# Kernel tuning notes

Hardware: AMD Instinct MI355X
Metric: run time of the kernel (lower is better)

Reference implementation:

```python
import jax, jax.numpy as jnp
import numpy as np

N_NODES = 50000
N_EDGES = 800000
IN_CH = 128
OUT_CH = 64
HID_CH = 2 * OUT_CH  # 128


def gcn_conv(x, edge_index, W, b, n_nodes):
    """PyG GCNConv: linear -> add self-loops -> sym-normalized scatter-add -> bias."""
    h = x @ W  # [N, out]
    loop = jnp.arange(n_nodes)
    row = jnp.concatenate([edge_index[0], loop])  # source nodes
    col = jnp.concatenate([edge_index[1], loop])  # target nodes
    deg = jax.ops.segment_sum(jnp.ones_like(col, dtype=h.dtype), col, num_segments=n_nodes)
    dinv = jnp.where(deg > 0, jax.lax.rsqrt(jnp.maximum(deg, 1.0)), 0.0)
    norm = dinv[row] * dinv[col]  # [E+N]
    msg = h[row] * norm[:, None]  # gather + scale, [E+N, out]
    out = jax.ops.segment_sum(msg, col, num_segments=n_nodes)  # scatter-add
    return out + b


def setup_inputs() -> dict:
    key = jax.random.key(0)
    ks = jax.random.split(key, 9)
    x = jax.random.normal(ks[0], (N_NODES, IN_CH), dtype=jnp.float32)
    edge_index = jax.random.randint(ks[1], (2, N_EDGES), 0, N_NODES, dtype=jnp.int64)
    s_in = 1.0 / np.sqrt(IN_CH)
    s_hid = 1.0 / np.sqrt(HID_CH)
    W1 = jax.random.normal(ks[2], (IN_CH, HID_CH), dtype=jnp.float32) * s_in
    b1 = jnp.zeros((HID_CH,), dtype=jnp.float32)
    W2 = jax.random.normal(ks[3], (HID_CH, OUT_CH), dtype=jnp.float32) * s_hid
    b2 = jnp.zeros((OUT_CH,), dtype=jnp.float32)
    W3 = jax.random.normal(ks[4], (HID_CH, OUT_CH), dtype=jnp.float32) * s_hid
    b3 = jnp.zeros((OUT_CH,), dtype=jnp.float32)
    return {"x": x, "edge_index": edge_index, "W1": W1, "b1": b1,
            "W2": W2, "b2": b2, "W3": W3, "b3": b3}


def reference(x, edge_index, W1, b1, W2, b2, W3, b3):
    act = jax.nn.relu
    hidden = act(gcn_conv(x, edge_index, W1, b1, N_NODES))
    x1 = act(gcn_conv(hidden, edge_index, W2, b2, N_NODES))
    x2 = act(gcn_conv(hidden, edge_index, W3, b3, N_NODES))
    return (x1, x2)
```

## Files before the change

### kernel.cpp

```cpp
#include <hip/hip_runtime.h>

#define N_NODES 50000
#define N_EDGES 800000
#define CH 128
#define SCAN_BLKS 98
#define WT_PAD 136
#define DUMMY N_NODES
#define AGG_HALF_BLKS 1563

typedef __attribute__((ext_vector_type(8))) short short8;
typedef __attribute__((ext_vector_type(4))) float floatx4;

__device__ __forceinline__ short f2bf(float f) {
    union { float f; unsigned u; } v; v.f = f;
    unsigned r = v.u + 0x7fff + ((v.u >> 16) & 1);
    return (short)(r >> 16);
}
__device__ __forceinline__ float bflo(unsigned u) {
    union { unsigned u; float f; } v; v.u = u << 16; return v.f;
}
__device__ __forceinline__ float bfhi(unsigned u) {
    union { unsigned u; float f; } v; v.u = u & 0xffff0000u; return v.f;
}


__global__ __launch_bounds__(256) void prep_kernel(const float* __restrict__ W1,
                                                   const float* __restrict__ W2,
                                                   const float* __restrict__ W3,
                                                   const float* __restrict__ b2,
                                                   const float* __restrict__ b3,
                                                   unsigned short* __restrict__ Wt1,
                                                   unsigned short* __restrict__ Wt23,
                                                   float* __restrict__ b23,
                                                   int* __restrict__ counts,
                                                   unsigned int* __restrict__ gdummy) {
    int i = blockIdx.x * blockDim.x + threadIdx.x;
    if (i < 128 * 128) {
        int n = i >> 7, k = i & 127;
        Wt1[i] = (unsigned short)f2bf(W1[k * 128 + n]);
        float w = (n < 64) ? W2[k * 64 + n] : W3[k * 64 + (n - 64)];
        Wt23[i] = (unsigned short)f2bf(w);
    } else if (i < 128 * 128 + 128) {
        int k2 = i - 128 * 128;
        b23[k2] = (k2 < 64) ? b2[k2] : b3[k2 - 64];
    } else if (i < 128 * 128 + 192) {
        gdummy[i - (128 * 128 + 128)] = 0;
    }
    for (int j = i; j < N_NODES; j += 66 * 256) counts[j] = 0;
}


__global__ void rank_kernel(const int* __restrict__ ei, int* __restrict__ counts,
                            int* __restrict__ rank) {
    int e = blockIdx.x * blockDim.x + threadIdx.x;
    if (e < N_EDGES) rank[e] = atomicAdd(&counts[ei[N_EDGES + e]], 1);
}

__global__ __launch_bounds__(256) void scan_block_kernel(const int* __restrict__ counts,
                                                         int* __restrict__ row_ptr,
                                                         float* __restrict__ dinv,
                                                         int* __restrict__ bsum) {
    __shared__ int s[256];
    int tid = threadIdx.x;
    int base = blockIdx.x * 512;
    int i0 = base + 2 * tid, i1 = i0 + 1;
    int v0 = (i0 < N_NODES) ? counts[i0] : 0;
    int v1 = (i1 < N_NODES) ? counts[i1] : 0;
    if (i0 < N_NODES) dinv[i0] = rsqrtf((float)(v0 + 1));
    if (i1 < N_NODES) dinv[i1] = rsqrtf((float)(v1 + 1));
    int p0 = (v0 + 3) & ~3, p1 = (v1 + 3) & ~3;
    int t = p0 + p1;
    s[tid] = t;
    __syncthreads();
    for (int off = 1; off < 256; off <<= 1) {
        int tmp = (tid >= off) ? s[tid - off] : 0;
        __syncthreads();
        s[tid] += tmp;
        __syncthreads();
    }
    int pre = s[tid] - t;
    if (i0 < N_NODES) row_ptr[i0] = pre;
    if (i1 < N_NODES) row_ptr[i1] = pre + p0;
    if (tid == 255) bsum[blockIdx.x] = s[255];
}

__global__ __launch_bounds__(256) void scan_fix_kernel(int* __restrict__ row_ptr,
                                                       const int* __restrict__ bsum,
                                                       const int* __restrict__ degs,
                                                       unsigned short* __restrict__ sorted_src) {
    __shared__ int s[128];
    int tid = threadIdx.x;
    if (tid < 128) s[tid] = (tid < SCAN_BLKS) ? bsum[tid] : 0;
    __syncthreads();
    for (int off = 1; off < 128; off <<= 1) {
        int t = (tid < 128 && tid >= off) ? s[tid - off] : 0;
        __syncthreads();
        if (tid < 128) s[tid] += t;
        __syncthreads();
    }
    int blockoff = (blockIdx.x == 0) ? 0 : s[blockIdx.x - 1];
    int base = blockIdx.x * 512;
    for (int i = base + tid; i < base + 512; i += 256) {
        if (i < N_NODES) {
            int v = row_ptr[i] + blockoff;
            row_ptr[i] = v;
            int d = degs[i];
            int pc = (d + 3) & ~3;
            for (int p = v + d; p < v + pc; ++p) sorted_src[p] = (unsigned short)DUMMY;
        }
    }
}

__global__ void scatter_plain(const int* __restrict__ ei, const int* __restrict__ row_ptr,
                              const int* __restrict__ rank,
                              unsigned short* __restrict__ sorted_src) {
    int e = blockIdx.x * blockDim.x + threadIdx.x;
    if (e < N_EDGES) {
        int dst = ei[N_EDGES + e];
        sorted_src[row_ptr[dst] + rank[e]] = (unsigned short)ei[e];
    }
}


template <bool A_BF16>
__global__ __launch_bounds__(256) void gemm_mfma(const void* __restrict__ Ain,
                                                 const unsigned short* __restrict__ Wt,
                                                 const float* __restrict__ dinv,
                                                 unsigned short* __restrict__ g) {
    __shared__ unsigned short lds[128 * WT_PAD];
    int tid = threadIdx.x;
    int wave = tid >> 6, lane = tid & 63;
    int quad = lane >> 4, ln = lane & 15;

    {
        int r = tid >> 1, h = tid & 1;
        const int4* src = (const int4*)(Wt + r * 128 + h * 64);
#pragma unroll
        for (int i = 0; i < 8; ++i)
            *(int4*)&lds[r * WT_PAD + h * 64 + i * 8] = src[i];
    }

    int row_base = blockIdx.x * 64 + wave * 16;
    int arow = row_base + ln;
    bool ok = arow < N_NODES;
    short8 afrag[4];
    if (A_BF16) {
        const unsigned short* A = (const unsigned short*)Ain;
#pragma unroll
        for (int kk = 0; kk < 4; ++kk) {
            short8 v = {};
            if (ok) v = *(const short8*)(A + arow * 128 + kk * 32 + quad * 8);
            afrag[kk] = v;
        }
    } else {
        const float* A = (const float*)Ain;
#pragma unroll
        for (int kk = 0; kk < 4; ++kk) {
            short8 v = {};
            if (ok) {
                const float* p = A + arow * 128 + kk * 32 + quad * 8;
#pragma unroll
                for (int j = 0; j < 8; ++j) v[j] = f2bf(p[j]);
            }
            afrag[kk] = v;
        }
    }
    __syncthreads();

    floatx4 acc[8] = {};
#pragma unroll
    for (int n0 = 0; n0 < 8; ++n0) {
#pragma unroll
        for (int kk = 0; kk < 4; ++kk) {
            short8 b = *(const short8*)&lds[(n0 * 16 + ln) * WT_PAD + kk * 32 + quad * 8];
            acc[n0] = __builtin_amdgcn_mfma_f32_16x16x32_bf16(afrag[kk], b, acc[n0], 0, 0, 0);
        }
    }

    __syncthreads();
    unsigned short* st = &lds[wave * 16 * WT_PAD];
    float dv[4];
#pragma unroll
    for (int r = 0; r < 4; ++r) {
        int node = row_base + quad * 4 + r;
        dv[r] = (node < N_NODES) ? dinv[node] : 0.f;
    }
#pragma unroll
    for (int n0 = 0; n0 < 8; ++n0)
#pragma unroll
        for (int r = 0; r < 4; ++r)
            st[(quad * 4 + r) * WT_PAD + n0 * 16 + ln] =
                (unsigned short)f2bf(acc[n0][r] * dv[r]);
    __syncthreads();

#pragma unroll
    for (int i = 0; i < 4; ++i) {
        int row = i * 4 + quad;
        int node = row_base + row;
        short8 v = *(const short8*)&st[row * WT_PAD + ln * 8];
        if (node < N_NODES) *(short8*)(g + node * 128 + ln * 8) = v;
    }
}


template <int MODE>
__global__ __launch_bounds__(256) void aggregate_bf16(const unsigned short* __restrict__ g,
                                                      const float* __restrict__ dinv,
                                                      const int* __restrict__ row_ptr,
                                                      const int* __restrict__ degs,
                                                      const unsigned short* __restrict__ srcs,
                                                      const float* __restrict__ bias,
                                                      void* __restrict__ outp) {
    int h = 0, nb = blockIdx.x;
    if (nb >= AGG_HALF_BLKS) { h = 1; nb -= AGG_HALF_BLKS; }
    int n = nb * 32 + (threadIdx.x >> 3);
    if (n >= N_NODES) return;
    int c4 = threadIdx.x & 7;
    int hoff = h * 8;
    const uint4* grow = (const uint4*)g;
    uint4 u = grow[n * 16 + hoff + c4];
    float a0 = bflo(u.x), a1 = bfhi(u.x), a2 = bflo(u.y), a3 = bfhi(u.y);
    float a4 = bflo(u.z), a5 = bfhi(u.z), a6 = bflo(u.w), a7 = bfhi(u.w);
    float c0 = 0.f, c1 = 0.f, c2 = 0.f, c3 = 0.f, c5 = 0.f, c6 = 0.f, c7 = 0.f, c8 = 0.f;
    int beg = row_ptr[n];
    int pend = beg + ((degs[n] + 3) & ~3);
    int e = beg;
    for (; e + 8 <= pend; e += 8) {
        ushort4 sa = *(const ushort4*)&srcs[e];
        ushort4 sb = *(const ushort4*)&srcs[e + 4];
        uint4 v0 = grow[sa.x * 16 + hoff + c4];
        uint4 v1 = grow[sa.y * 16 + hoff + c4];
        uint4 v2 = grow[sa.z * 16 + hoff + c4];
        uint4 v3 = grow[sa.w * 16 + hoff + c4];
        uint4 v4 = grow[sb.x * 16 + hoff + c4];
        uint4 v5 = grow[sb.y * 16 + hoff + c4];
        uint4 v6 = grow[sb.z * 16 + hoff + c4];
        uint4 v7 = grow[sb.w * 16 + hoff + c4];
        a0 += bflo(v0.x); a1 += bfhi(v0.x); a2 += bflo(v0.y); a3 += bfhi(v0.y);
        a4 += bflo(v0.z); a5 += bfhi(v0.z); a6 += bflo(v0.w); a7 += bfhi(v0.w);
        c0 += bflo(v1.x); c1 += bfhi(v1.x); c2 += bflo(v1.y); c3 += bfhi(v1.y);
        c5 += bflo(v1.z); c6 += bfhi(v1.z); c7 += bflo(v1.w); c8 += bfhi(v1.w);
        a0 += bflo(v2.x); a1 += bfhi(v2.x); a2 += bflo(v2.y); a3 += bfhi(v2.y);
        a4 += bflo(v2.z); a5 += bfhi(v2.z); a6 += bflo(v2.w); a7 += bfhi(v2.w);
        c0 += bflo(v3.x); c1 += bfhi(v3.x); c2 += bflo(v3.y); c3 += bfhi(v3.y);
        c5 += bflo(v3.z); c6 += bfhi(v3.z); c7 += bflo(v3.w); c8 += bfhi(v3.w);
        a0 += bflo(v4.x); a1 += bfhi(v4.x); a2 += bflo(v4.y); a3 += bfhi(v4.y);
        a4 += bflo(v4.z); a5 += bfhi(v4.z); a6 += bflo(v4.w); a7 += bfhi(v4.w);
        c0 += bflo(v5.x); c1 += bfhi(v5.x); c2 += bflo(v5.y); c3 += bfhi(v5.y);
        c5 += bflo(v5.z); c6 += bfhi(v5.z); c7 += bflo(v5.w); c8 += bfhi(v5.w);
        a0 += bflo(v6.x); a1 += bfhi(v6.x); a2 += bflo(v6.y); a3 += bfhi(v6.y);
        a4 += bflo(v6.z); a5 += bfhi(v6.z); a6 += bflo(v6.w); a7 += bfhi(v6.w);
        c0 += bflo(v7.x); c1 += bfhi(v7.x); c2 += bflo(v7.y); c3 += bfhi(v7.y);
        c5 += bflo(v7.z); c6 += bfhi(v7.z); c7 += bflo(v7.w); c8 += bfhi(v7.w);
    }
    if (e < pend) {
        ushort4 sa = *(const ushort4*)&srcs[e];
        uint4 v0 = grow[sa.x * 16 + hoff + c4];
        uint4 v1 = grow[sa.y * 16 + hoff + c4];
        uint4 v2 = grow[sa.z * 16 + hoff + c4];
        uint4 v3 = grow[sa.w * 16 + hoff + c4];
        a0 += bflo(v0.x); a1 += bfhi(v0.x); a2 += bflo(v0.y); a3 += bfhi(v0.y);
        a4 += bflo(v0.z); a5 += bfhi(v0.z); a6 += bflo(v0.w); a7 += bfhi(v0.w);
        c0 += bflo(v1.x); c1 += bfhi(v1.x); c2 += bflo(v1.y); c3 += bfhi(v1.y);
        c5 += bflo(v1.z); c6 += bfhi(v1.z); c7 += bflo(v1.w); c8 += bfhi(v1.w);
        a0 += bflo(v2.x); a1 += bfhi(v2.x); a2 += bflo(v2.y); a3 += bfhi(v2.y);
        a4 += bflo(v2.z); a5 += bfhi(v2.z); a6 += bflo(v2.w); a7 += bfhi(v2.w);
        c0 += bflo(v3.x); c1 += bfhi(v3.x); c2 += bflo(v3.y); c3 += bfhi(v3.y);
        c5 += bflo(v3.z); c6 += bfhi(v3.z); c7 += bflo(v3.w); c8 += bfhi(v3.w);
    }
    a0 += c0; a1 += c1; a2 += c2; a3 += c3; a4 += c5; a5 += c6; a6 += c7; a7 += c8;
    float d = dinv[n];
    float4 bv0 = ((const float4*)bias)[h * 16 + c4 * 2];
    float4 bv1 = ((const float4*)bias)[h * 16 + c4 * 2 + 1];
    float o0 = fmaxf(d * a0 + bv0.x, 0.f);
    float o1 = fmaxf(d * a1 + bv0.y, 0.f);
    float o2 = fmaxf(d * a2 + bv0.z, 0.f);
    float o3 = fmaxf(d * a3 + bv0.w, 0.f);
    float o4 = fmaxf(d * a4 + bv1.x, 0.f);
    float o5 = fmaxf(d * a5 + bv1.y, 0.f);
    float o6 = fmaxf(d * a6 + bv1.z, 0.f);
    float o7 = fmaxf(d * a7 + bv1.w, 0.f);
    if (MODE == 0) {
        uint4 w;
        w.x = ((unsigned)(unsigned short)f2bf(o0)) | (((unsigned)(unsigned short)f2bf(o1)) << 16);
        w.y = ((unsigned)(unsigned short)f2bf(o2)) | (((unsigned)(unsigned short)f2bf(o3)) << 16);
        w.z = ((unsigned)(unsigned short)f2bf(o4)) | (((unsigned)(unsigned short)f2bf(o5)) << 16);
        w.w = ((unsigned)(unsigned short)f2bf(o6)) | (((unsigned)(unsigned short)f2bf(o7)) << 16);
        ((uint4*)outp)[n * 16 + hoff + c4] = w;
    } else {
        float* out = (float*)outp + (size_t)h * N_NODES * 64;
        ((float4*)out)[n * 16 + c4 * 2] = make_float4(o0, o1, o2, o3);
        ((float4*)out)[n * 16 + c4 * 2 + 1] = make_float4(o4, o5, o6, o7);
    }
}


extern "C" void kernel_launch(void* const* d_in, const int* in_sizes, int n_in,
                              void* d_out, int out_size, void* d_ws, size_t ws_size,
                              hipStream_t stream) {
    const float* x  = (const float*)d_in[0];
    const int*   ei = (const int*)d_in[1];
    const float* W1 = (const float*)d_in[2];
    const float* b1 = (const float*)d_in[3];
    const float* W2 = (const float*)d_in[4];
    const float* b2 = (const float*)d_in[5];
    const float* W3 = (const float*)d_in[6];
    const float* b3 = (const float*)d_in[7];
    float* out = (float*)d_out;

    char* w = (char*)d_ws;
    int*            counts     = (int*)(w + 0);
    int*            row_ptr    = (int*)(w + 204800);
    float*          dinv       = (float*)(w + 409600);
    int*            rank       = (int*)(w + 614400);
    unsigned short* sorted_src = (unsigned short*)(w + 3814400);
    unsigned short* Wt1        = (unsigned short*)(w + 7614400);
    unsigned short* Wt23       = (unsigned short*)(w + 7647168);
    float*          b23        = (float*)(w + 7679936);
    int*            bsum       = (int*)(w + 7680448);
    unsigned short* g1         = (unsigned short*)(w + 8388608);
    unsigned short* hidden     = (unsigned short*)(w + 22020096);

    prep_kernel<<<66, 256, 0, stream>>>(W1, W2, W3, b2, b3, Wt1, Wt23, b23, counts,
                                        (unsigned int*)(g1 + N_NODES * 128));
    rank_kernel<<<(N_EDGES + 255) / 256, 256, 0, stream>>>(ei, counts, rank);
    scan_block_kernel<<<SCAN_BLKS, 256, 0, stream>>>(counts, row_ptr, dinv, bsum);
    scan_fix_kernel<<<SCAN_BLKS, 256, 0, stream>>>(row_ptr, bsum, counts, sorted_src);
    scatter_plain<<<(N_EDGES + 255) / 256, 256, 0, stream>>>(ei, row_ptr, rank, sorted_src);

    const int gemm_blocks = (N_NODES + 63) / 64;
    const int agg_blocks = 2 * AGG_HALF_BLKS;

    gemm_mfma<false><<<gemm_blocks, 256, 0, stream>>>(x, Wt1, dinv, g1);
    aggregate_bf16<0><<<agg_blocks, 256, 0, stream>>>(g1, dinv, row_ptr, counts, sorted_src, b1, hidden);

    gemm_mfma<true><<<gemm_blocks, 256, 0, stream>>>(hidden, Wt23, dinv, g1);
    aggregate_bf16<1><<<agg_blocks, 256, 0, stream>>>(g1, dinv, row_ptr, counts, sorted_src, b23, out);
}
```

Measured before the change: 217.3 us.

## Fuse layer-1 aggregation with layer-2/3 GEMM and split final aggregation into quarters

The first aggregation now writes its ReLU'd bf16 hidden rows into an LDS tile, and the same block immediately runs the MFMA GEMM against the combined W2|W3 weights. This removes the hidden tensor's global write and re-read and drops one kernel launch. The final aggregation is split over a 2D grid of 32-channel quarters with 4 threads per node. The fused kernel uses 4 threads per node with 32 float accumulators each and a simple 2-edge loop, which raises register pressure and lowers gather parallelism compared with the former 8-edge unrolled loop.

New measurement: 245.4 us. +12.9%, slower.

```diff
diff --git a/kernel.cpp b/kernel.cpp
--- a/kernel.cpp
+++ b/kernel.cpp
@@ -6,7 +6,6 @@
 #define SCAN_BLKS 98
 #define WT_PAD 136
 #define DUMMY N_NODES
-#define AGG_HALF_BLKS 1563
 
 typedef __attribute__((ext_vector_type(8))) short short8;
 typedef __attribute__((ext_vector_type(4))) float floatx4;
@@ -21,6 +20,15 @@
 }
 __device__ __forceinline__ float bfhi(unsigned u) {
     union { unsigned u; float f; } v; v.u = u & 0xffff0000u; return v.f;
+}
+__device__ __forceinline__ unsigned packbf(float a, float b) {
+    return ((unsigned)(unsigned short)f2bf(a)) | (((unsigned)(unsigned short)f2bf(b)) << 16);
+}
+__device__ __forceinline__ void acc8(float* a, uint4 v) {
+    a[0] += bflo(v.x); a[1] += bfhi(v.x);
+    a[2] += bflo(v.y); a[3] += bfhi(v.y);
+    a[4] += bflo(v.z); a[5] += bfhi(v.z);
+    a[6] += bflo(v.w); a[7] += bfhi(v.w);
 }
 
 
@@ -33,7 +41,8 @@
                                                    unsigned short* __restrict__ Wt23,
                                                    float* __restrict__ b23,
                                                    int* __restrict__ counts,
-                                                   unsigned int* __restrict__ gdummy) {
+                                                   unsigned int* __restrict__ g1dummy,
+                                                   unsigned int* __restrict__ g2dummy) {
     int i = blockIdx.x * blockDim.x + threadIdx.x;
     if (i < 128 * 128) {
         int n = i >> 7, k = i & 127;
@@ -44,7 +53,9 @@
         int k2 = i - 128 * 128;
         b23[k2] = (k2 < 64) ? b2[k2] : b3[k2 - 64];
     } else if (i < 128 * 128 + 192) {
-        gdummy[i - (128 * 128 + 128)] = 0;
+        g1dummy[i - (128 * 128 + 128)] = 0;
+    } else if (i < 128 * 128 + 256) {
+        g2dummy[i - (128 * 128 + 192)] = 0;
     }
     for (int j = i; j < N_NODES; j += 66 * 256) counts[j] = 0;
 }
@@ -122,11 +133,10 @@
 }
 
 
-template <bool A_BF16>
-__global__ __launch_bounds__(256) void gemm_mfma(const void* __restrict__ Ain,
-                                                 const unsigned short* __restrict__ Wt,
-                                                 const float* __restrict__ dinv,
-                                                 unsigned short* __restrict__ g) {
+__global__ __launch_bounds__(256) void gemm_mfma_f32(const float* __restrict__ A,
+                                                     const unsigned short* __restrict__ Wt,
+                                                     const float* __restrict__ dinv,
+                                                     unsigned short* __restrict__ g) {
     __shared__ unsigned short lds[128 * WT_PAD];
     int tid = threadIdx.x;
     int wave = tid >> 6, lane = tid & 63;
@@ -144,26 +154,15 @@
     int arow = row_base + ln;
     bool ok = arow < N_NODES;
     short8 afrag[4];
-    if (A_BF16) {
-        const unsigned short* A = (const unsigned short*)Ain;
-#pragma unroll
-        for (int kk = 0; kk < 4; ++kk) {
-            short8 v = {};
-            if (ok) v = *(const short8*)(A + arow * 128 + kk * 32 + quad * 8);
-            afrag[kk] = v;
-        }
-    } else {
-        const float* A = (const float*)Ain;
-#pragma unroll
-        for (int kk = 0; kk < 4; ++kk) {
-            short8 v = {};
-            if (ok) {
-                const float* p = A + arow * 128 + kk * 32 + quad * 8;
-#pragma unroll
-                for (int j = 0; j < 8; ++j) v[j] = f2bf(p[j]);
-            }
-            afrag[kk] = v;
-        }
+#pragma unroll
+    for (int kk = 0; kk < 4; ++kk) {
+        short8 v = {};
+        if (ok) {
+            const float* p = A + arow * 128 + kk * 32 + quad * 8;
+#pragma unroll
+            for (int j = 0; j < 8; ++j) v[j] = f2bf(p[j]);
+        }
+        afrag[kk] = v;
     }
     __syncthreads();
 
@@ -203,95 +202,181 @@
 }
 
 
-template <int MODE>
-__global__ __launch_bounds__(256) void aggregate_bf16(const unsigned short* __restrict__ g,
+__global__ __launch_bounds__(256) void agg_gemm_fused(const unsigned short* __restrict__ g1,
                                                       const float* __restrict__ dinv,
                                                       const int* __restrict__ row_ptr,
                                                       const int* __restrict__ degs,
                                                       const unsigned short* __restrict__ srcs,
-                                                      const float* __restrict__ bias,
-                                                      void* __restrict__ outp) {
-    int h = 0, nb = blockIdx.x;
-    if (nb >= AGG_HALF_BLKS) { h = 1; nb -= AGG_HALF_BLKS; }
-    int n = nb * 32 + (threadIdx.x >> 3);
+                                                      const float* __restrict__ b1,
+                                                      const unsigned short* __restrict__ Wt23,
+                                                      unsigned short* __restrict__ g2) {
+    __shared__ unsigned short wlds[128 * WT_PAD];
+    __shared__ unsigned short atile[64 * WT_PAD];
+    int tid = threadIdx.x;
+
+    {
+        int r = tid >> 1, h = tid & 1;
+        const int4* src = (const int4*)(Wt23 + r * 128 + h * 64);
+#pragma unroll
+        for (int i = 0; i < 8; ++i)
+            *(int4*)&wlds[r * WT_PAD + h * 64 + i * 8] = src[i];
+    }
+
+    int slot = tid >> 2;
+    int part = tid & 3;
+    int n = blockIdx.x * 64 + slot;
+    unsigned short* arow = &atile[slot * WT_PAD + part * 32];
+    if (n < N_NODES) {
+        const uint4* grow = (const uint4*)g1;
+        const uint4* gr = grow + (size_t)n * 16 + part * 4;
+        float acc[32];
+        {
+            uint4 u0 = gr[0], u1 = gr[1], u2 = gr[2], u3 = gr[3];
+#pragma unroll
+            for (int j = 0; j < 32; ++j) acc[j] = 0.f;
+            acc8(acc, u0); acc8(acc + 8, u1); acc8(acc + 16, u2); acc8(acc + 24, u3);
+        }
+        int beg = row_ptr[n];
+        int pend = beg + ((degs[n] + 3) & ~3);
+        for (int e = beg; e < pend; e += 2) {
+            ushort2 ss = *(const ushort2*)&srcs[e];
+            const uint4* p0 = grow + (size_t)ss.x * 16 + part * 4;
+            const uint4* p1 = grow + (size_t)ss.y * 16 + part * 4;
+            uint4 va0 = p0[0], va1 = p0[1], va2 = p0[2], va3 = p0[3];
+            uint4 vb0 = p1[0], vb1 = p1[1], vb2 = p1[2], vb3 = p1[3];
+            acc8(acc, va0); acc8(acc + 8, va1); acc8(acc + 16, va2); acc8(acc + 24, va3);
+            acc8(acc, vb0); acc8(acc + 8, vb1); acc8(acc + 16, vb2); acc8(acc + 24, vb3);
+        }
+        float d = dinv[n];
+        const float4* bb = (const float4*)b1 + part * 8;
+        unsigned wbuf[16];
+#pragma unroll
+        for (int j = 0; j < 8; ++j) {
+            float4 b = bb[j];
+            float o0 = fmaxf(d * acc[4 * j + 0] + b.x, 0.f);
+            float o1 = fmaxf(d * acc[4 * j + 1] + b.y, 0.f);
+            float o2 = fmaxf(d * acc[4 * j + 2] + b.z, 0.f);
+            float o3 = fmaxf(d * acc[4 * j + 3] + b.w, 0.f);
+            wbuf[2 * j] = packbf(o0, o1);
+            wbuf[2 * j + 1] = packbf(o2, o3);
+        }
+#pragma unroll
+        for (int j = 0; j < 4; ++j)
+            *(int4*)(arow + j * 8) = *(const int4*)&wbuf[j * 4];
+    } else {
+        int4 z = {0, 0, 0, 0};
+#pragma unroll
+        for (int j = 0; j < 4; ++j) *(int4*)(arow + j * 8) = z;
+    }
+    __syncthreads();
+
+    int wave = tid >> 6, lane = tid & 63;
+    int quad = lane >> 4, ln = lane & 15;
+    int row_base = blockIdx.x * 64 + wave * 16;
+    short8 afrag[4];
+#pragma unroll
+    for (int kk = 0; kk < 4; ++kk)
+        afrag[kk] = *(const short8*)&atile[(wave * 16 + ln) * WT_PAD + kk * 32 + quad * 8];
+
+    floatx4 acc2[8] = {};
+#pragma unroll
+    for (int n0 = 0; n0 < 8; ++n0) {
+#pragma unroll
+        for (int kk = 0; kk < 4; ++kk) {
+            short8 b = *(const short8*)&wlds[(n0 * 16 + ln) * WT_PAD + kk * 32 + quad * 8];
+            acc2[n0] = __builtin_amdgcn_mfma_f32_16x16x32_bf16(afrag[kk], b, acc2[n0], 0, 0, 0);
+        }
+    }
+
+    __syncthreads();
+    unsigned short* st = &wlds[wave * 16 * WT_PAD];
+    float dv[4];
+#pragma unroll
+    for (int r = 0; r < 4; ++r) {
+        int node = row_base + quad * 4 + r;
+        dv[r] = (node < N_NODES) ? dinv[node] : 0.f;
+    }
+#pragma unroll
+    for (int n0 = 0; n0 < 8; ++n0)
+#pragma unroll
+        for (int r = 0; r < 4; ++r)
+            st[(quad * 4 + r) * WT_PAD + n0 * 16 + ln] =
+                (unsigned short)f2bf(acc2[n0][r] * dv[r]);
+    __syncthreads();
+
+#pragma unroll
+    for (int i = 0; i < 4; ++i) {
+        int row = i * 4 + quad;
+        int node = row_base + row;
+        short8 v = *(const short8*)&st[row * WT_PAD + ln * 8];
+        if (node < N_NODES) *(short8*)(g2 + node * 128 + ln * 8) = v;
+    }
+}
+
+
+__global__ __launch_bounds__(256) void aggregate_q(const unsigned short* __restrict__ g,
+                                                   const float* __restrict__ dinv,
+                                                   const int* __restrict__ row_ptr,
+                                                   const int* __restrict__ degs,
+                                                   const unsigned short* __restrict__ srcs,
+                                                   const float* __restrict__ bias,
+                                                   float* __restrict__ out) {
+    int q = blockIdx.y;
+    int n = blockIdx.x * 64 + (threadIdx.x >> 2);
     if (n >= N_NODES) return;
-    int c4 = threadIdx.x & 7;
-    int hoff = h * 8;
+    int c4 = threadIdx.x & 3;
+    int qoff = q * 4 + c4;
     const uint4* grow = (const uint4*)g;
-    uint4 u = grow[n * 16 + hoff + c4];
-    float a0 = bflo(u.x), a1 = bfhi(u.x), a2 = bflo(u.y), a3 = bfhi(u.y);
-    float a4 = bflo(u.z), a5 = bfhi(u.z), a6 = bflo(u.w), a7 = bfhi(u.w);
-    float c0 = 0.f, c1 = 0.f, c2 = 0.f, c3 = 0.f, c5 = 0.f, c6 = 0.f, c7 = 0.f, c8 = 0.f;
+    float a[8], c[8];
+    {
+        uint4 u = grow[(size_t)n * 16 + qoff];
+        a[0] = bflo(u.x); a[1] = bfhi(u.x); a[2] = bflo(u.y); a[3] = bfhi(u.y);
+        a[4] = bflo(u.z); a[5] = bfhi(u.z); a[6] = bflo(u.w); a[7] = bfhi(u.w);
+#pragma unroll
+        for (int j = 0; j < 8; ++j) c[j] = 0.f;
+    }
     int beg = row_ptr[n];
     int pend = beg + ((degs[n] + 3) & ~3);
     int e = beg;
     for (; e + 8 <= pend; e += 8) {
         ushort4 sa = *(const ushort4*)&srcs[e];
         ushort4 sb = *(const ushort4*)&srcs[e + 4];
-        uint4 v0 = grow[sa.x * 16 + hoff + c4];
-        uint4 v1 = grow[sa.y * 16 + hoff + c4];
-        uint4 v2 = grow[sa.z * 16 + hoff + c4];
-        uint4 v3 = grow[sa.w * 16 + hoff + c4];
-        uint4 v4 = grow[sb.x * 16 + hoff + c4];
-        uint4 v5 = grow[sb.y * 16 + hoff + c4];
-        uint4 v6 = grow[sb.z * 16 + hoff + c4];
-        uint4 v7 = grow[sb.w * 16 + hoff + c4];
-        a0 += bflo(v0.x); a1 += bfhi(v0.x); a2 += bflo(v0.y); a3 += bfhi(v0.y);
-        a4 += bflo(v0.z); a5 += bfhi(v0.z); a6 += bflo(v0.w); a7 += bfhi(v0.w);
-        c0 += bflo(v1.x); c1 += bfhi(v1.x); c2 += bflo(v1.y); c3 += bfhi(v1.y);
-        c5 += bflo(v1.z); c6 += bfhi(v1.z); c7 += bflo(v1.w); c8 += bfhi(v1.w);
-        a0 += bflo(v2.x); a1 += bfhi(v2.x); a2 += bflo(v2.y); a3 += bfhi(v2.y);
-        a4 += bflo(v2.z); a5 += bfhi(v2.z); a6 += bflo(v2.w); a7 += bfhi(v2.w);
-        c0 += bflo(v3.x); c1 += bfhi(v3.x); c2 += bflo(v3.y); c3 += bfhi(v3.y);
-        c5 += bflo(v3.z); c6 += bfhi(v3.z); c7 += bflo(v3.w); c8 += bfhi(v3.w);
-        a0 += bflo(v4.x); a1 += bfhi(v4.x); a2 += bflo(v4.y); a3 += bfhi(v4.y);
-        a4 += bflo(v4.z); a5 += bfhi(v4.z); a6 += bflo(v4.w); a7 += bfhi(v4.w);
-        c0 += bflo(v5.x); c1 += bfhi(v5.x); c2 += bflo(v5.y); c3 += bfhi(v5.y);
-        c5 += bflo(v5.z); c6 += bfhi(v5.z); c7 += bflo(v5.w); c8 += bfhi(v5.w);
-        a0 += bflo(v6.x); a1 += bfhi(v6.x); a2 += bflo(v6.y); a3 += bfhi(v6.y);
-        a4 += bflo(v6.z); a5 += bfhi(v6.z); a6 += bflo(v6.w); a7 += bfhi(v6.w);
-        c0 += bflo(v7.x); c1 += bfhi(v7.x); c2 += bflo(v7.y); c3 += bfhi(v7.y);
-        c5 += bflo(v7.z); c6 += bfhi(v7.z); c7 += bflo(v7.w); c8 += bfhi(v7.w);
+        uint4 v0 = grow[(size_t)sa.x * 16 + qoff];
+        uint4 v1 = grow[(size_t)sa.y * 16 + qoff];
+        uint4 v2 = grow[(size_t)sa.z * 16 + qoff];
+        uint4 v3 = grow[(size_t)sa.w * 16 + qoff];
+        uint4 v4 = grow[(size_t)sb.x * 16 + qoff];
+        uint4 v5 = grow[(size_t)sb.y * 16 + qoff];
+        uint4 v6 = grow[(size_t)sb.z * 16 + qoff];
+        uint4 v7 = grow[(size_t)sb.w * 16 + qoff];
+        acc8(a, v0); acc8(c, v1); acc8(a, v2); acc8(c, v3);
+        acc8(a, v4); acc8(c, v5); acc8(a, v6); acc8(c, v7);
     }
     if (e < pend) {
         ushort4 sa = *(const ushort4*)&srcs[e];
-        uint4 v0 = grow[sa.x * 16 + hoff + c4];
-        uint4 v1 = grow[sa.y * 16 + hoff + c4];
-        uint4 v2 = grow[sa.z * 16 + hoff + c4];
-        uint4 v3 = grow[sa.w * 16 + hoff + c4];
-        a0 += bflo(v0.x); a1 += bfhi(v0.x); a2 += bflo(v0.y); a3 += bfhi(v0.y);
-        a4 += bflo(v0.z); a5 += bfhi(v0.z); a6 += bflo(v0.w); a7 += bfhi(v0.w);
-        c0 += bflo(v1.x); c1 += bfhi(v1.x); c2 += bflo(v1.y); c3 += bfhi(v1.y);
-        c5 += bflo(v1.z); c6 += bfhi(v1.z); c7 += bflo(v1.w); c8 += bfhi(v1.w);
-        a0 += bflo(v2.x); a1 += bfhi(v2.x); a2 += bflo(v2.y); a3 += bfhi(v2.y);
-        a4 += bflo(v2.z); a5 += bfhi(v2.z); a6 += bflo(v2.w); a7 += bfhi(v2.w);
-        c0 += bflo(v3.x); c1 += bfhi(v3.x); c2 += bflo(v3.y); c3 += bfhi(v3.y);
-        c5 += bflo(v3.z); c6 += bfhi(v3.z); c7 += bflo(v3.w); c8 += bfhi(v3.w);
-    }
-    a0 += c0; a1 += c1; a2 += c2; a3 += c3; a4 += c5; a5 += c6; a6 += c7; a7 += c8;
+        uint4 v0 = grow[(size_t)sa.x * 16 + qoff];
+        uint4 v1 = grow[(size_t)sa.y * 16 + qoff];
+        uint4 v2 = grow[(size_t)sa.z * 16 + qoff];
+        uint4 v3 = grow[(size_t)sa.w * 16 + qoff];
+        acc8(a, v0); acc8(c, v1); acc8(a, v2); acc8(c, v3);
+    }
+#pragma unroll
+    for (int j = 0; j < 8; ++j) a[j] += c[j];
     float d = dinv[n];
-    float4 bv0 = ((const float4*)bias)[h * 16 + c4 * 2];
-    float4 bv1 = ((const float4*)bias)[h * 16 + c4 * 2 + 1];
-    float o0 = fmaxf(d * a0 + bv0.x, 0.f);
-    float o1 = fmaxf(d * a1 + bv0.y, 0.f);
-    float o2 = fmaxf(d * a2 + bv0.z, 0.f);
-    float o3 = fmaxf(d * a3 + bv0.w, 0.f);
-    float o4 = fmaxf(d * a4 + bv1.x, 0.f);
-    float o5 = fmaxf(d * a5 + bv1.y, 0.f);
-    float o6 = fmaxf(d * a6 + bv1.z, 0.f);
-    float o7 = fmaxf(d * a7 + bv1.w, 0.f);
-    if (MODE == 0) {
-        uint4 w;
-        w.x = ((unsigned)(unsigned short)f2bf(o0)) | (((unsigned)(unsigned short)f2bf(o1)) << 16);
-        w.y = ((unsigned)(unsigned short)f2bf(o2)) | (((unsigned)(unsigned short)f2bf(o3)) << 16);
-        w.z = ((unsigned)(unsigned short)f2bf(o4)) | (((unsigned)(unsigned short)f2bf(o5)) << 16);
-        w.w = ((unsigned)(unsigned short)f2bf(o6)) | (((unsigned)(unsigned short)f2bf(o7)) << 16);
-        ((uint4*)outp)[n * 16 + hoff + c4] = w;
-    } else {
-        float* out = (float*)outp + (size_t)h * N_NODES * 64;
-        ((float4*)out)[n * 16 + c4 * 2] = make_float4(o0, o1, o2, o3);
-        ((float4*)out)[n * 16 + c4 * 2 + 1] = make_float4(o4, o5, o6, o7);
-    }
+    float4 bv0 = ((const float4*)bias)[q * 8 + c4 * 2];
+    float4 bv1 = ((const float4*)bias)[q * 8 + c4 * 2 + 1];
+    float4 p0, p1;
+    p0.x = fmaxf(d * a[0] + bv0.x, 0.f);
+    p0.y = fmaxf(d * a[1] + bv0.y, 0.f);
+    p0.z = fmaxf(d * a[2] + bv0.z, 0.f);
+    p0.w = fmaxf(d * a[3] + bv0.w, 0.f);
+    p1.x = fmaxf(d * a[4] + bv1.x, 0.f);
+    p1.y = fmaxf(d * a[5] + bv1.y, 0.f);
+    p1.z = fmaxf(d * a[6] + bv1.z, 0.f);
+    p1.w = fmaxf(d * a[7] + bv1.w, 0.f);
+    float* ob = out + (size_t)(q >> 1) * N_NODES * 64 + n * 64 + (q & 1) * 32 + c4 * 8;
+    *(float4*)ob = p0;
+    *(float4*)(ob + 4) = p1;
 }
 
 
@@ -319,21 +404,23 @@
     float*          b23        = (float*)(w + 7679936);
     int*            bsum       = (int*)(w + 7680448);
     unsigned short* g1         = (unsigned short*)(w + 8388608);
-    unsigned short* hidden     = (unsigned short*)(w + 22020096);
+    unsigned short* g2         = (unsigned short*)(w + 22020096);
 
     prep_kernel<<<66, 256, 0, stream>>>(W1, W2, W3, b2, b3, Wt1, Wt23, b23, counts,
-                                        (unsigned int*)(g1 + N_NODES * 128));
+                                        (unsigned int*)(g1 + N_NODES * 128),
+                                        (unsigned int*)(g2 + N_NODES * 128));
     rank_kernel<<<(N_EDGES + 255) / 256, 256, 0, stream>>>(ei, counts, rank);
     scan_block_kernel<<<SCAN_BLKS, 256, 0, stream>>>(counts, row_ptr, dinv, bsum);
     scan_fix_kernel<<<SCAN_BLKS, 256, 0, stream>>>(row_ptr, bsum, counts, sorted_src);
     scatter_plain<<<(N_EDGES + 255) / 256, 256, 0, stream>>>(ei, row_ptr, rank, sorted_src);
 
-    const int gemm_blocks = (N_NODES + 63) / 64;
-    const int agg_blocks = 2 * AGG_HALF_BLKS;
-
-    gemm_mfma<false><<<gemm_blocks, 256, 0, stream>>>(x, Wt1, dinv, g1);
-    aggregate_bf16<0><<<agg_blocks, 256, 0, stream>>>(g1, dinv, row_ptr, counts, sorted_src, b1, hidden);
-
-    gemm_mfma<true><<<gemm_blocks, 256, 0, stream>>>(hidden, Wt23, dinv, g1);
-    aggregate_bf16<1><<<agg_blocks, 256, 0, stream>>>(g1, dinv, row_ptr, counts, sorted_src, b23, out);
-}
+    const int tile_blocks = (N_NODES + 63) / 64;
+
+    gemm_mfma_f32<<<tile_blocks, 256, 0, stream>>>(x, Wt1, dinv, g1);
+
+    agg_gemm_fused<<<tile_blocks, 256, 0, stream>>>(g1, dinv, row_ptr, counts, sorted_src,
+                                                    b1, Wt23, g2);
+
+    aggregate_q<<<dim3(tile_blocks, 4), 256, 0, stream>>>(g2, dinv, row_ptr, counts,
+                                                          sorted_src, b23, out);
+}
```
